# Kernel tuning notes

Hardware: AMD Instinct MI355X
Metric: run time of the kernel (lower is better)

Reference implementation:

```python
import jax, jax.numpy as jnp
import numpy as np

K = 8          # num groups / object slots
FC = 256       # fc_size
LAST = 128     # last_fc_size
B = 2048       # batch
M = 1024       # input size
H = 512        # state (hidden) size


def _ln(x, g, b):
    # LayerNorm over last dim, eps matches torch default 1e-5
    mu = jnp.mean(x, axis=-1, keepdims=True)
    var = jnp.mean((x - mu) ** 2, axis=-1, keepdims=True)
    return (x - mu) * jax.lax.rsqrt(var + 1e-5) * g + b


def setup_inputs() -> dict:
    key = jax.random.key(0)
    ks = jax.random.split(key, 10)
    s = 0.05
    d = {
        "x": jax.random.normal(ks[0], (B * K, M), jnp.float32),
        "state": jax.random.normal(ks[1], (B * K, H), jnp.float32),
        # encoder: Linear(H->FC) + LN(FC)
        "enc_w": jax.random.normal(ks[2], (H, FC), jnp.float32) * s,
        "enc_b": jnp.zeros((FC,), jnp.float32),
        "enc_g": jnp.ones((FC,), jnp.float32),
        "enc_bb": jnp.zeros((FC,), jnp.float32),
        # core: Linear(2*FC->FC) + LN(FC)
        "core_w": jax.random.normal(ks[3], (2 * FC, FC), jnp.float32) * s,
        "core_b": jnp.zeros((FC,), jnp.float32),
        "core_g": jnp.ones((FC,), jnp.float32),
        "core_bb": jnp.zeros((FC,), jnp.float32),
        # context: Linear(FC->FC) + LN(FC)
        "ctx_w": jax.random.normal(ks[4], (FC, FC), jnp.float32) * s,
        "ctx_b": jnp.zeros((FC,), jnp.float32),
        "ctx_g": jnp.ones((FC,), jnp.float32),
        "ctx_bb": jnp.zeros((FC,), jnp.float32),
        # attention: Linear(FC->LAST) + LN(LAST) + Tanh + Linear(LAST->1) + Sigmoid
        "att1_w": jax.random.normal(ks[5], (FC, LAST), jnp.float32) * s,
        "att1_b": jnp.zeros((LAST,), jnp.float32),
        "att_g": jnp.ones((LAST,), jnp.float32),
        "att_bb": jnp.zeros((LAST,), jnp.float32),
        "att2_w": jax.random.normal(ks[6], (LAST, 1), jnp.float32) * s,
        "att2_b": jnp.zeros((1,), jnp.float32),
        # out_fc: Linear(FC + FC + M -> FC)
        "out_w": jax.random.normal(ks[7], (FC + FC + M, FC), jnp.float32) * s,
        "out_b": jnp.zeros((FC,), jnp.float32),
    }
    return d


def reference(x, state, enc_w, enc_b, enc_g, enc_bb,
              core_w, core_b, core_g, core_bb,
              ctx_w, ctx_b, ctx_g, ctx_bb,
              att1_w, att1_b, att_g, att_bb, att2_w, att2_b,
              out_w, out_b):
    bk, m = x.shape
    k = K
    b = bk // k
    # 0. encode state: [B*K, H] -> [B*K, FC]
    s1 = jax.nn.relu(_ln(state @ enc_w + enc_b, enc_g, enc_bb))
    h1 = s1.shape[-1]
    s1r = s1.reshape(b, k, h1)
    # focus: K-1 copies of each slot's state  [b, k, k-1, h1]
    fs = jnp.broadcast_to(s1r[:, :, None, :], (b, k, k - 1, h1))
    # context: gather the K-1 other slots' states (replaces torch python loop)
    idx = np.array([[j for j in range(k) if j != i] for i in range(k)])  # [k, k-1]
    cs = s1r[:, idx, :]  # [b, k, k-1, h1]
    concat = jnp.concatenate([fs, cs], axis=-1).reshape(b * k * (k - 1), 2 * h1)
    # core / context MLPs over pairs
    core = jax.nn.relu(_ln(concat @ core_w + core_b, core_g, core_bb))   # [b*k*(k-1), FC]
    ctx = jax.nn.relu(_ln(core @ ctx_w + ctx_b, ctx_g, ctx_bb))          # [b*k*(k-1), FC]
    # attention scalar per pair
    att_h = jnp.tanh(_ln(core @ att1_w + att1_b, att_g, att_bb))
    att = jax.nn.sigmoid(att_h @ att2_w + att2_b)                        # [b*k*(k-1), 1]
    # attention-weighted sum over the K-1 context dim
    h2 = ctx.shape[-1]
    effect = jnp.sum(ctx.reshape(b * k, k - 1, h2) * att.reshape(b * k, k - 1, 1), axis=1)
    # decode: concat encoded state, effect, input -> new state
    total = jnp.concatenate([s1, effect, x], axis=-1)
    new_state = total @ out_w + out_b
    return (new_state, new_state)
```

## Files before the change

kernel.cpp:

```cpp
#include <hip/hip_runtime.h>
#include <stdint.h>

#define FC    256
#define HH    512
#define MX    1024
#define LASTN 128
#define NROW  16384
#define NGRP  2048

typedef unsigned short u16;
typedef __bf16 bf16x8 __attribute__((ext_vector_type(8)));
typedef float  f32x4  __attribute__((ext_vector_type(4)));

__device__ __forceinline__ float red16(float v) {
#pragma unroll
  for (int m = 1; m < 16; m <<= 1) v += __shfl_xor(v, m);
  return v;
}
__device__ __forceinline__ float red16hi(float v) {
#pragma unroll
  for (int m = 4; m < 64; m <<= 1) v += __shfl_xor(v, m);
  return v;
}
__device__ __forceinline__ u16 to_bf16(float f) {
  unsigned u = __float_as_uint(f);
  return (u16)((u + 0x8000u) >> 16);
}
__device__ __forceinline__ float from_bf16(u16 s) {
  return __uint_as_float(((unsigned)s) << 16);
}
__device__ __forceinline__ uint32_t pk2(float a, float b) {
  return (uint32_t)to_bf16(a) | ((uint32_t)to_bf16(b) << 16);
}
__device__ __forceinline__ float tanh_fast(float x) {
  float e = __expf(2.f * x);
  return __fdividef(e - 1.f, e + 1.f);
}
__device__ __forceinline__ float sigmoid_fast(float x) {
  return __fdividef(1.f, 1.f + __expf(-x));
}
__device__ __forceinline__ void glds16(const void* g, void* l) {
  __builtin_amdgcn_global_load_lds(
      (__attribute__((address_space(1))) uint32_t*)g,
      (__attribute__((address_space(3))) uint32_t*)l, 16, 0, 0);
}
__device__ __forceinline__ bf16x8 frag_ld(const u16* p) {
  return __builtin_bit_cast(bf16x8, *(const uint4*)p);
}

__global__ __launch_bounds__(256) void k_prep(
    const float* __restrict__ enc_w, const float* __restrict__ core_w,
    const float* __restrict__ ctx_w, const float* __restrict__ att1_w,
    const float* __restrict__ out_w,
    u16* __restrict__ encT, u16* __restrict__ uvT, u16* __restrict__ ctxT,
    u16* __restrict__ attT, u16* __restrict__ outT)
{
  const int bx = blockIdx.x, tid = threadIdx.x;
  const float* W; u16* D; int NKC, N, local; int uv = 0;
  if (bx < 64)       { W = enc_w;  D = encT; NKC = 16; N = 256; local = bx * 256 + tid; }
  else if (bx < 128) { W = core_w; D = uvT;  NKC = 8;  N = 256; local = (bx-64)*256 + tid; uv = 1; }
  else if (bx < 160) { W = ctx_w;  D = ctxT; NKC = 8;  N = 256; local = (bx-128)*256 + tid; }
  else if (bx < 176) { W = att1_w; D = attT; NKC = 8;  N = 128; local = (bx-160)*256 + tid; }
  else               { W = out_w;  D = outT; NKC = 48; N = 256; local = (bx-176)*256 + tid; }
  const int l  = local & 63;
  const int kc = (local >> 6) % NKC;
  const int u  = (local >> 6) / NKC;
  const int n  = u * 16 + (l & 15);
  const int k0 = kc * 32 + (l >> 4) * 8;
  float f[8];
#pragma unroll
  for (int j = 0; j < 8; ++j) {
    const int k = k0 + j;
    if (uv) f[j] = (n < 256) ? W[(size_t)k * 256 + n] : W[(size_t)(256 + k) * 256 + (n - 256)];
    else    f[j] = W[(size_t)k * N + n];
  }
  uint4 w;
  w.x = pk2(f[0], f[1]); w.y = pk2(f[2], f[3]);
  w.z = pk2(f[4], f[5]); w.w = pk2(f[6], f[7]);
  *(uint4*)&D[(size_t)local * 8] = w;
}

__global__ __launch_bounds__(256) void k_enc(
    const float* __restrict__ state, const u16* __restrict__ encT,
    const float* __restrict__ enc_b, const float* __restrict__ enc_g,
    const float* __restrict__ enc_bb, u16* __restrict__ s1b)
{
  __shared__ __align__(16) u16 smA[2][128 * 8];
  __shared__ __align__(16) u16 smB[2][16 * 64 * 8];
  __shared__ float smP[2][2][16][2];
  const int tid = threadIdx.x, wv = tid >> 6, lane = tid & 63;
  const int cl = lane & 15, quad = lane >> 4;
  const int rb = wv >> 1, cb = wv & 1;
  const int row0 = blockIdx.x * 32;
  f32x4 acc[8];
#pragma unroll
  for (int u = 0; u < 8; ++u) acc[u] = (f32x4){0.f, 0.f, 0.f, 0.f};

  for (int kk = 0; kk < 8; ++kk) {
    __syncthreads();
    {
      const int p = tid >> 7, lu = tid & 127;
      const int kc = kk * 2 + p;
      const int rblk = lu >> 6, ll = lu & 63;
      const float* src = state + (size_t)(row0 + rblk * 16 + (ll & 15)) * HH + kc * 32 + (ll >> 4) * 8;
      float4 a = *(const float4*)src, b = *(const float4*)(src + 4);
      uint4 w; w.x = pk2(a.x, a.y); w.y = pk2(a.z, a.w); w.z = pk2(b.x, b.y); w.w = pk2(b.z, b.w);
      *(uint4*)&smA[p][(size_t)lu * 8] = w;
    }
#pragma unroll
    for (int p = 0; p < 2; ++p)
#pragma unroll
      for (int i = 0; i < 4; ++i) {
        const int u = wv * 4 + i;
        glds16(encT + ((size_t)(u * 16 + kk * 2 + p) * 64 + lane) * 8, &smB[p][u * 512]);
      }
    __syncthreads();
#pragma unroll
    for (int p = 0; p < 2; ++p) {
      bf16x8 af = frag_ld(&smA[p][(rb * 64 + lane) * 8]);
#pragma unroll
      for (int u = 0; u < 8; ++u) {
        bf16x8 bf = frag_ld(&smB[p][((cb * 8 + u) * 64 + lane) * 8]);
        acc[u] = __builtin_amdgcn_mfma_f32_16x16x32_bf16(af, bf, acc[u], 0, 0, 0);
      }
    }
  }
  float bias[8], gg[8], bb[8];
#pragma unroll
  for (int u = 0; u < 8; ++u) {
    const int col = cb * 128 + u * 16 + cl;
    bias[u] = enc_b[col]; gg[u] = enc_g[col]; bb[u] = enc_bb[col];
  }
  float vv[4][8];
#pragma unroll
  for (int r4 = 0; r4 < 4; ++r4) {
    float s = 0.f, sq = 0.f;
#pragma unroll
    for (int u = 0; u < 8; ++u) {
      float v = acc[u][r4] + bias[u];
      vv[r4][u] = v; s += v; sq += v * v;
    }
    s = red16(s); sq = red16(sq);
    if (cl == 0) { smP[cb][rb][quad * 4 + r4][0] = s; smP[cb][rb][quad * 4 + r4][1] = sq; }
  }
  __syncthreads();
#pragma unroll
  for (int r4 = 0; r4 < 4; ++r4) {
    const int rr = quad * 4 + r4;
    const float S  = smP[0][rb][rr][0] + smP[1][rb][rr][0];
    const float SQ = smP[0][rb][rr][1] + smP[1][rb][rr][1];
    const float mu = S * (1.f / 256.f);
    const float rs = rsqrtf(SQ * (1.f / 256.f) - mu * mu + 1e-5f);
    const int row = row0 + rb * 16 + rr;
#pragma unroll
    for (int u = 0; u < 8; ++u) {
      float o = fmaxf((vv[r4][u] - mu) * rs * gg[u] + bb[u], 0.f);
      s1b[(size_t)row * FC + cb * 128 + u * 16 + cl] = to_bf16(o);
    }
  }
}

__global__ __launch_bounds__(256) void k_uv(
    const u16* __restrict__ s1b, const u16* __restrict__ uvT,
    float* __restrict__ UV)
{
  __shared__ __align__(16) u16 smA[2][4 * 64 * 8];
  __shared__ __align__(16) u16 smB[2][8 * 64 * 8];
  const int tid = threadIdx.x, wv = tid >> 6, lane = tid & 63;
  const int cl = lane & 15, quad = lane >> 4;
  const int row0 = blockIdx.x * 64;
  const int nb = blockIdx.y;
  f32x4 acc[8];
#pragma unroll
  for (int u = 0; u < 8; ++u) acc[u] = (f32x4){0.f, 0.f, 0.f, 0.f};

  for (int kk = 0; kk < 4; ++kk) {
    __syncthreads();
#pragma unroll
    for (int p = 0; p < 2; ++p) {
      const int kc = kk * 2 + p;
      glds16(s1b + (size_t)(row0 + wv * 16 + (lane & 15)) * FC + kc * 32 + (lane >> 4) * 8,
             &smA[p][wv * 512]);
#pragma unroll
      for (int i = 0; i < 2; ++i) {
        const int u = wv * 2 + i;
        glds16(uvT + ((size_t)((nb * 8 + u) * 8 + kc) * 64 + lane) * 8, &smB[p][u * 512]);
      }
    }
    __syncthreads();
#pragma unroll
    for (int p = 0; p < 2; ++p) {
      bf16x8 af = frag_ld(&smA[p][(wv * 64 + lane) * 8]);
#pragma unroll
      for (int u = 0; u < 8; ++u) {
        bf16x8 bf = frag_ld(&smB[p][(u * 64 + lane) * 8]);
        acc[u] = __builtin_amdgcn_mfma_f32_16x16x32_bf16(af, bf, acc[u], 0, 0, 0);
      }
    }
  }
#pragma unroll
  for (int r4 = 0; r4 < 4; ++r4) {
    const int row = row0 + wv * 16 + quad * 4 + r4;
#pragma unroll
    for (int u = 0; u < 8; ++u)
      UV[(size_t)row * 512 + nb * 128 + u * 16 + cl] = acc[u][r4];
  }
}

__global__ __launch_bounds__(256, 3) void k_pair(
    const float* __restrict__ UV, const float* __restrict__ core_b,
    const float* __restrict__ core_g, const float* __restrict__ core_bb,
    const u16* __restrict__ ctxT, const float* __restrict__ ctx_b,
    const float* __restrict__ ctx_g, const float* __restrict__ ctx_bb,
    const u16* __restrict__ attT, const float* __restrict__ att1_b,
    const float* __restrict__ att_g, const float* __restrict__ att_bb,
    const float* __restrict__ att2_w, const float* __restrict__ att2_b,
    u16* __restrict__ effb)
{
  __shared__ __align__(16) u16 smA[2048 * 8];
  __shared__ __align__(16) u16 smX[16 * 64 * 8];
  __shared__ float att_s[64];
  float* smUV = (float*)smX;
  u16*   smB  = smX;
  const int g = blockIdx.x;
  const int tid = threadIdx.x, wv = tid >> 6, lane = tid & 63;
  const int cl = lane & 15, quad = lane >> 4;
  const int aswz = ((lane >> 5) & 1) << 2;

#pragma unroll
  for (int i = 0; i < 4; ++i) {
    const int r = wv * 4 + i;
    const int row = g * 8 + (r & 7);
    const int half = r >> 3;
    glds16(UV + (size_t)row * 512 + half * 256 + lane * 4, &smUV[r * 256]);
  }
#pragma unroll
  for (int i = 0; i < 8; ++i)
    *(uint4*)&smA[(size_t)(tid + i * 256) * 8] = (uint4){0u, 0u, 0u, 0u};
  __syncthreads();

  {
    const int s4  = lane & 3;
    const int g16 = lane >> 2;
    const int c0  = g16 * 16;
    float4 CB[4], CG[4], CBB[4];
#pragma unroll
    for (int q = 0; q < 4; ++q) {
      const int cq = c0 + ((q ^ s4) << 2);
      CB[q]  = *(const float4*)&core_b[cq];
      CG[q]  = *(const float4*)&core_g[cq];
      CBB[q] = *(const float4*)&core_bb[cq];
    }
#pragma unroll
    for (int it = 0; it < 4; ++it) {
      const int p = it * 16 + wv * 4 + s4;
      if (p < 56) {
        const int i = p / 7, t = p - i * 7;
        const int j = t + (t >= i ? 1 : 0);
        const float* uA = &smUV[i * 256 + c0];
        const float* vB = &smUV[(8 + j) * 256 + c0];
        float v[16];
        float s = 0.f, sq = 0.f;
#pragma unroll
        for (int q = 0; q < 4; ++q) {
          const int qo = (q ^ s4) << 2;
          float4 ua = *(const float4*)(uA + qo);
          float4 vb = *(const float4*)(vB + qo);
          float x0 = ua.x + vb.x + CB[q].x, x1 = ua.y + vb.y + CB[q].y;
          float x2 = ua.z + vb.z + CB[q].z, x3 = ua.w + vb.w + CB[q].w;
          v[q*4+0] = x0; v[q*4+1] = x1; v[q*4+2] = x2; v[q*4+3] = x3;
          s += x0 + x1 + x2 + x3;
          sq += x0*x0 + x1*x1 + x2*x2 + x3*x3;
        }
        s = red16hi(s); sq = red16hi(sq);
        const float mu = s * (1.f / 256.f);
        const float rs = rsqrtf(sq * (1.f / 256.f) - mu * mu + 1e-5f);
#pragma unroll
        for (int q = 0; q < 4; ++q) {
          v[q*4+0] = fmaxf((v[q*4+0] - mu) * rs * CG[q].x + CBB[q].x, 0.f);
          v[q*4+1] = fmaxf((v[q*4+1] - mu) * rs * CG[q].y + CBB[q].y, 0.f);
          v[q*4+2] = fmaxf((v[q*4+2] - mu) * rs * CG[q].z + CBB[q].z, 0.f);
          v[q*4+3] = fmaxf((v[q*4+3] - mu) * rs * CG[q].w + CBB[q].w, 0.f);
        }
#pragma unroll
        for (int q = 0; q < 4; ++q) {
          const int lg = q ^ s4;
          const int ks = (g16 * 2 + (lg >> 1)) & 3;
          int slot = ((p >> 4) * 8 + (g16 >> 1)) * 64 + (p & 15) + 16 * ks;
          slot ^= ((slot >> 5) & 1) << 2;
          uint2 w;
          w.x = pk2(v[q*4+0], v[q*4+1]);
          w.y = pk2(v[q*4+2], v[q*4+3]);
          *(uint2*)&smA[(size_t)slot * 8 + (lg & 1) * 4] = w;
        }
      }
    }
  }
  __syncthreads();

  f32x4 accT[8];
#pragma unroll
  for (int t = 0; t < 8; ++t) accT[t] = (f32x4){0.f, 0.f, 0.f, 0.f};
#pragma unroll 2
  for (int kc = 0; kc < 8; ++kc) {
    uint4 attf[8];
#pragma unroll
    for (int q = 0; q < 8; ++q)
      attf[q] = *(const uint4*)(attT + ((size_t)(q * 8 + kc) * 64 + lane) * 8);
    bf16x8 af = frag_ld(&smA[(size_t)((((wv * 8 + kc) * 64) + lane) ^ aswz) * 8]);
#pragma unroll
    for (int q = 0; q < 8; ++q) {
      bf16x8 bf = __builtin_bit_cast(bf16x8, attf[q]);
      accT[q] = __builtin_amdgcn_mfma_f32_16x16x32_bf16(af, bf, accT[q], 0, 0, 0);
    }
  }

#pragma unroll
  for (int i = 0; i < 4; ++i) {
    const int q = wv * 4 + i;
    glds16(ctxT + ((size_t)(q * 8 + 0) * 64 + lane) * 8, &smB[q * 512]);
  }

  {
    float ab[8], ag[8], abb[8], aw[8];
#pragma unroll
    for (int t = 0; t < 8; ++t) {
      const int col = t * 16 + cl;
      ab[t] = att1_b[col]; ag[t] = att_g[col]; abb[t] = att_bb[col]; aw[t] = att2_w[col];
    }
    const float b2 = att2_b[0];
#pragma unroll
    for (int r4 = 0; r4 < 4; ++r4) {
      float v[8], s = 0.f, sq = 0.f;
#pragma unroll
      for (int t = 0; t < 8; ++t) {
        v[t] = accT[t][r4] + ab[t];
        s += v[t]; sq += v[t] * v[t];
      }
      s = red16(s); sq = red16(sq);
      const float mu = s * (1.f / 128.f);
      const float rs = rsqrtf(sq * (1.f / 128.f) - mu * mu + 1e-5f);
      float d = 0.f;
#pragma unroll
      for (int t = 0; t < 8; ++t) {
        float h = tanh_fast((v[t] - mu) * rs * ag[t] + abb[t]);
        d = fmaf(h, aw[t], d);
      }
      d = red16(d);
      if (cl == 0) {
        const int r = wv * 16 + quad * 4 + r4;
        if (r < 56) att_s[r] = sigmoid_fast(d + b2);
      }
    }
  }

  f32x4 accC[16];
#pragma unroll
  for (int t = 0; t < 16; ++t) accC[t] = (f32x4){0.f, 0.f, 0.f, 0.f};
  for (int kc = 0; kc < 8; ++kc) {
    __syncthreads();
    bf16x8 af = frag_ld(&smA[(size_t)((((wv * 8 + kc) * 64) + lane) ^ aswz) * 8]);
#pragma unroll
    for (int q = 0; q < 16; ++q) {
      bf16x8 bf = frag_ld(&smB[(q * 64 + lane) * 8]);
      accC[q] = __builtin_amdgcn_mfma_f32_16x16x32_bf16(af, bf, accC[q], 0, 0, 0);
    }
    __syncthreads();
    if (kc < 7) {
#pragma unroll
      for (int i = 0; i < 4; ++i) {
        const int q = wv * 4 + i;
        glds16(ctxT + ((size_t)(q * 8 + kc + 1) * 64 + lane) * 8, &smB[q * 512]);
      }
    }
  }

  u16* smS = smA;
  {
    float cb[16], cg[16], cbb[16];
#pragma unroll
    for (int t = 0; t < 16; ++t) {
      const int col = t * 16 + cl;
      cb[t] = ctx_b[col]; cg[t] = ctx_g[col]; cbb[t] = ctx_bb[col];
    }
#pragma unroll
    for (int r4 = 0; r4 < 4; ++r4) {
      float v[16], s = 0.f, sq = 0.f;
#pragma unroll
      for (int t = 0; t < 16; ++t) {
        v[t] = accC[t][r4] + cb[t];
        s += v[t]; sq += v[t] * v[t];
      }
      s = red16(s); sq = red16(sq);
      const float mu = s * (1.f / 256.f);
      const float rs = rsqrtf(sq * (1.f / 256.f) - mu * mu + 1e-5f);
      const int r = wv * 16 + quad * 4 + r4;
      if (r < 56) {
        const float ap = att_s[r];
#pragma unroll
        for (int t = 0; t < 16; ++t) {
          const int col = t * 16 + cl;
          float o = fmaxf((v[t] - mu) * rs * cg[t] + cbb[t], 0.f) * ap;
          smS[r * 264 + col] = to_bf16(o);
        }
      }
    }
  }
  __syncthreads();

  const int c = tid;
#pragma unroll
  for (int i = 0; i < 8; ++i) {
    float s = 0.f;
#pragma unroll
    for (int t2 = 0; t2 < 7; ++t2) s += from_bf16(smS[(i * 7 + t2) * 264 + c]);
    effb[(size_t)(g * 8 + i) * FC + c] = to_bf16(s);
  }
}

__global__ __launch_bounds__(256) void k_out(
    const u16* __restrict__ s1b, const u16* __restrict__ effb,
    const float* __restrict__ x, const u16* __restrict__ outT,
    const float* __restrict__ out_b, float* __restrict__ out, int dup)
{
  __shared__ __align__(16) u16 smA[2][4 * 64 * 8];
  __shared__ __align__(16) u16 smB[2][8 * 64 * 8];
  const int tid = threadIdx.x, wv = tid >> 6, lane = tid & 63;
  const int cl = lane & 15, quad = lane >> 4;
  const int row0 = blockIdx.x * 64;
  const int nb = blockIdx.y;
  f32x4 acc[8];
#pragma unroll
  for (int u = 0; u < 8; ++u) acc[u] = (f32x4){0.f, 0.f, 0.f, 0.f};

  for (int kk = 0; kk < 24; ++kk) {
    const int kc0 = kk * 2;
    __syncthreads();
    if (kc0 < 16) {
#pragma unroll
      for (int p = 0; p < 2; ++p) {
        const int kc = kc0 + p;
        const u16* base = (kc < 8) ? s1b : effb;
        const int kof = (kc & 7) * 32;
        glds16(base + (size_t)(row0 + wv * 16 + (lane & 15)) * FC + kof + (lane >> 4) * 8,
               &smA[p][wv * 512]);
      }
    } else {
      const int t = tid >> 6, ll = tid & 63;
      const float* src0 = x + (size_t)(row0 + t * 16 + (ll & 15)) * MX + (ll >> 4) * 8;
#pragma unroll
      for (int p = 0; p < 2; ++p) {
        const float* src = src0 + (kc0 + p - 16) * 32;
        float4 a = *(const float4*)src, b = *(const float4*)(src + 4);
        uint4 w; w.x = pk2(a.x, a.y); w.y = pk2(a.z, a.w); w.z = pk2(b.x, b.y); w.w = pk2(b.z, b.w);
        *(uint4*)&smA[p][(size_t)tid * 8] = w;
      }
    }
#pragma unroll
    for (int p = 0; p < 2; ++p)
#pragma unroll
      for (int i = 0; i < 2; ++i) {
        const int u = wv * 2 + i;
        glds16(outT + ((size_t)((nb * 8 + u) * 48 + kc0 + p) * 64 + lane) * 8, &smB[p][u * 512]);
      }
    __syncthreads();
#pragma unroll
    for (int p = 0; p < 2; ++p) {
      bf16x8 af = frag_ld(&smA[p][(wv * 64 + lane) * 8]);
#pragma unroll
      for (int u = 0; u < 8; ++u) {
        bf16x8 bf = frag_ld(&smB[p][(u * 64 + lane) * 8]);
        acc[u] = __builtin_amdgcn_mfma_f32_16x16x32_bf16(af, bf, acc[u], 0, 0, 0);
      }
    }
  }
  float bias[8];
#pragma unroll
  for (int u = 0; u < 8; ++u) bias[u] = out_b[nb * 128 + u * 16 + cl];
#pragma unroll
  for (int r4 = 0; r4 < 4; ++r4) {
    const int row = row0 + wv * 16 + quad * 4 + r4;
#pragma unroll
    for (int u = 0; u < 8; ++u) {
      const float o = acc[u][r4] + bias[u];
      const size_t off = (size_t)row * FC + nb * 128 + u * 16 + cl;
      out[off] = o;
      if (dup) out[(size_t)NROW * FC + off] = o;
    }
  }
}

extern "C" void kernel_launch(void* const* d_in, const int* in_sizes, int n_in,
                              void* d_out, int out_size, void* d_ws, size_t ws_size,
                              hipStream_t stream) {
  const float* x      = (const float*)d_in[0];
  const float* state  = (const float*)d_in[1];
  const float* enc_w  = (const float*)d_in[2];
  const float* enc_b  = (const float*)d_in[3];
  const float* enc_g  = (const float*)d_in[4];
  const float* enc_bb = (const float*)d_in[5];
  const float* core_w = (const float*)d_in[6];
  const float* core_b = (const float*)d_in[7];
  const float* core_g = (const float*)d_in[8];
  const float* core_bb= (const float*)d_in[9];
  const float* ctx_w  = (const float*)d_in[10];
  const float* ctx_b  = (const float*)d_in[11];
  const float* ctx_g  = (const float*)d_in[12];
  const float* ctx_bb = (const float*)d_in[13];
  const float* att1_w = (const float*)d_in[14];
  const float* att1_b = (const float*)d_in[15];
  const float* att_g  = (const float*)d_in[16];
  const float* att_bb = (const float*)d_in[17];
  const float* att2_w = (const float*)d_in[18];
  const float* att2_b = (const float*)d_in[19];
  const float* out_w  = (const float*)d_in[20];
  const float* out_b  = (const float*)d_in[21];

  char* ws = (char*)d_ws;
  float* UV  = (float*)ws;
  u16* s1b   = (u16*)(ws + 33554432);
  u16* effb  = (u16*)(ws + 41943040);
  u16* encT  = (u16*)(ws + 50331648);
  u16* uvT   = (u16*)(ws + 50593792);
  u16* ctxT  = (u16*)(ws + 50855936);
  u16* attT  = (u16*)(ws + 50987008);
  u16* outT  = (u16*)(ws + 51052544);
  float* out = (float*)d_out;
  const int dup = (out_size >= 2 * NROW * FC) ? 1 : 0;

  k_prep<<<dim3(368), 256, 0, stream>>>(enc_w, core_w, ctx_w, att1_w, out_w,
                                        encT, uvT, ctxT, attT, outT);
  k_enc<<<dim3(NROW / 32), 256, 0, stream>>>(state, encT, enc_b, enc_g, enc_bb, s1b);
  k_uv <<<dim3(NROW / 64, 4), 256, 0, stream>>>(s1b, uvT, UV);
  k_pair<<<dim3(NGRP), 256, 0, stream>>>(UV, core_b, core_g, core_bb,
                                         ctxT, ctx_b, ctx_g, ctx_bb,
                                         attT, att1_b, att_g, att_bb,
                                         att2_w, att2_b, effb);
  k_out<<<dim3(NROW / 64, 2), 256, 0, stream>>>(s1b, effb, x, outT, out_b, out, dup);
}
```

Measured before the change: 287.3 us.

## Retile output GEMM to full-width column tiles so x is read once

```diff
diff --git a/kernel.cpp b/kernel.cpp
--- a/kernel.cpp
+++ b/kernel.cpp
@@ -423,12 +423,13 @@
     const float* __restrict__ x, const u16* __restrict__ outT,
     const float* __restrict__ out_b, float* __restrict__ out, int dup)
 {
-  __shared__ __align__(16) u16 smA[2][4 * 64 * 8];
-  __shared__ __align__(16) u16 smB[2][8 * 64 * 8];
+  __shared__ __align__(16) u16 smA[2][2 * 64 * 8];
+  __shared__ __align__(16) u16 smB[2][16 * 64 * 8];
   const int tid = threadIdx.x, wv = tid >> 6, lane = tid & 63;
   const int cl = lane & 15, quad = lane >> 4;
-  const int row0 = blockIdx.x * 64;
-  const int nb = blockIdx.y;
+  const int row0 = blockIdx.x * 32;
+  const int rw = wv >> 1;
+  const int cw = wv & 1;
   f32x4 acc[8];
 #pragma unroll
   for (int u = 0; u < 8; ++u) acc[u] = (f32x4){0.f, 0.f, 0.f, 0.f};
@@ -437,53 +438,50 @@
     const int kc0 = kk * 2;
     __syncthreads();
     if (kc0 < 16) {
-#pragma unroll
-      for (int p = 0; p < 2; ++p) {
-        const int kc = kc0 + p;
-        const u16* base = (kc < 8) ? s1b : effb;
-        const int kof = (kc & 7) * 32;
-        glds16(base + (size_t)(row0 + wv * 16 + (lane & 15)) * FC + kof + (lane >> 4) * 8,
-               &smA[p][wv * 512]);
-      }
+      const int p = wv >> 1, u = wv & 1;
+      const int kc = kc0 + p;
+      const u16* base = (kc < 8) ? s1b : effb;
+      const int kof = (kc & 7) * 32;
+      glds16(base + (size_t)(row0 + u * 16 + (lane & 15)) * FC + kof + (lane >> 4) * 8,
+             &smA[p][u * 512]);
     } else {
-      const int t = tid >> 6, ll = tid & 63;
-      const float* src0 = x + (size_t)(row0 + t * 16 + (ll & 15)) * MX + (ll >> 4) * 8;
-#pragma unroll
-      for (int p = 0; p < 2; ++p) {
-        const float* src = src0 + (kc0 + p - 16) * 32;
-        float4 a = *(const float4*)src, b = *(const float4*)(src + 4);
-        uint4 w; w.x = pk2(a.x, a.y); w.y = pk2(a.z, a.w); w.z = pk2(b.x, b.y); w.w = pk2(b.z, b.w);
-        *(uint4*)&smA[p][(size_t)tid * 8] = w;
-      }
+      const int p = tid >> 7, lu = tid & 127;
+      const int kc = kc0 + p;
+      const int u = lu >> 6, l = lu & 63;
+      const float* src = x + (size_t)(row0 + u * 16 + (l & 15)) * MX
+                           + (kc - 16) * 32 + (l >> 4) * 8;
+      float4 a = *(const float4*)src, b = *(const float4*)(src + 4);
+      uint4 w; w.x = pk2(a.x, a.y); w.y = pk2(a.z, a.w); w.z = pk2(b.x, b.y); w.w = pk2(b.z, b.w);
+      *(uint4*)&smA[p][(size_t)(u * 64 + l) * 8] = w;
     }
 #pragma unroll
     for (int p = 0; p < 2; ++p)
 #pragma unroll
-      for (int i = 0; i < 2; ++i) {
-        const int u = wv * 2 + i;
-        glds16(outT + ((size_t)((nb * 8 + u) * 48 + kc0 + p) * 64 + lane) * 8, &smB[p][u * 512]);
+      for (int i = 0; i < 4; ++i) {
+        const int u = wv * 4 + i;
+        glds16(outT + ((size_t)(u * 48 + kc0 + p) * 64 + lane) * 8, &smB[p][u * 512]);
       }
     __syncthreads();
 #pragma unroll
     for (int p = 0; p < 2; ++p) {
-      bf16x8 af = frag_ld(&smA[p][(wv * 64 + lane) * 8]);
-#pragma unroll
-      for (int u = 0; u < 8; ++u) {
-        bf16x8 bf = frag_ld(&smB[p][(u * 64 + lane) * 8]);
-        acc[u] = __builtin_amdgcn_mfma_f32_16x16x32_bf16(af, bf, acc[u], 0, 0, 0);
+      bf16x8 af = frag_ld(&smA[p][(rw * 64 + lane) * 8]);
+#pragma unroll
+      for (int i = 0; i < 8; ++i) {
+        bf16x8 bf = frag_ld(&smB[p][((cw * 8 + i) * 64 + lane) * 8]);
+        acc[i] = __builtin_amdgcn_mfma_f32_16x16x32_bf16(af, bf, acc[i], 0, 0, 0);
       }
     }
   }
   float bias[8];
 #pragma unroll
-  for (int u = 0; u < 8; ++u) bias[u] = out_b[nb * 128 + u * 16 + cl];
+  for (int i = 0; i < 8; ++i) bias[i] = out_b[cw * 128 + i * 16 + cl];
 #pragma unroll
   for (int r4 = 0; r4 < 4; ++r4) {
-    const int row = row0 + wv * 16 + quad * 4 + r4;
-#pragma unroll
-    for (int u = 0; u < 8; ++u) {
-      const float o = acc[u][r4] + bias[u];
-      const size_t off = (size_t)row * FC + nb * 128 + u * 16 + cl;
+    const int row = row0 + rw * 16 + quad * 4 + r4;
+#pragma unroll
+    for (int i = 0; i < 8; ++i) {
+      const float o = acc[i][r4] + bias[i];
+      const size_t off = (size_t)row * FC + cw * 128 + i * 16 + cl;
       out[off] = o;
       if (dup) out[(size_t)NROW * FC + off] = o;
     }
@@ -536,5 +534,5 @@
                                          ctxT, ctx_b, ctx_g, ctx_bb,
                                          attT, att1_b, att_g, att_bb,
                                          att2_w, att2_b, effb);
-  k_out<<<dim3(NROW / 64, 2), 256, 0, stream>>>(s1b, effb, x, outT, out_b, out, dup);
-}
+  k_out<<<dim3(NROW / 32), 256, 0, stream>>>(s1b, effb, x, outT, out_b, out, dup);
+}
```

After: 285.7 us. About the same (-0.6%).
